# Optimization experiments

Measured on AMD Instinct MI355X. Metric: run time of the kernel, lower is better.

## Reference

```python
import jax, jax.numpy as jnp
import numpy as np
import math

B, T, F, H = 8, 1024, 512, 8
D = F // H  # 64
MIN_VAL = float(np.finfo(np.float32).min)


def setup_inputs() -> dict:
    key = jax.random.key(0)
    ks = jax.random.split(key, 16)
    w = lambda k, shape: jax.random.normal(k, shape, dtype=jnp.float32) * 0.02
    return {
        "query": jax.random.normal(ks[0], (B, T, F), dtype=jnp.float32),
        "key": jax.random.normal(ks[1], (B, T, F), dtype=jnp.float32),
        "value": jax.random.normal(ks[2], (B, T, F), dtype=jnp.float32),
        "mask": jax.random.randint(ks[3], (B, T, T), 0, 2, dtype=jnp.int32),
        "pos_emb": jax.random.normal(ks[4], (1, T, F), dtype=jnp.float32),
        "Wq": w(ks[5], (F, F)), "bq": jnp.zeros((F,), jnp.float32),
        "Wk": w(ks[6], (F, F)), "bk": jnp.zeros((F,), jnp.float32),
        "Wv": w(ks[7], (F, F)), "bv": jnp.zeros((F,), jnp.float32),
        "Wp": w(ks[8], (F, F)),
        "Wo": w(ks[9], (F, F)), "bo": jnp.zeros((F,), jnp.float32),
        "pos_bias_u": w(ks[10], (H, D)),
        "pos_bias_v": w(ks[11], (H, D)),
    }


def reference(query, key, value, mask, pos_emb, Wq, bq, Wk, bk, Wv, bv, Wp, Wo, bo, pos_bias_u, pos_bias_v):
    n_batch = query.shape[0]
    # projections (torch Linear: x @ W.T + b)
    q = (query @ Wq.T + bq).reshape(n_batch, -1, H, D)          # (B, T1, H, D)
    k = (key @ Wk.T + bk).reshape(n_batch, -1, H, D).transpose(0, 2, 1, 3)    # (B, H, T2, D)
    v = (value @ Wv.T + bv).reshape(n_batch, -1, H, D).transpose(0, 2, 1, 3)  # (B, H, T2, D)
    # relative position projection; pos_emb batch is 1 -> squeeze for broadcast
    p = (pos_emb @ Wp.T).reshape(pos_emb.shape[0], -1, H, D).transpose(0, 2, 1, 3)[0]  # (H, T2, D)

    q_u = q + pos_bias_u  # broadcast (H, D) over (B, T1, H, D)
    q_v = q + pos_bias_v
    matrix_ac = jnp.einsum("bthd,bhsd->bhts", q_u, k)
    matrix_bd = jnp.einsum("bthd,hsd->bhts", q_v, p)
    scores = (matrix_ac + matrix_bd) / math.sqrt(D)  # (B, H, T1, T2)

    m = (mask[:, None, :, :] == 0)  # (B, 1, T1, T2)
    scores = jnp.where(m, MIN_VAL, scores)
    attn = jnp.where(m, 0.0, jax.nn.softmax(scores, axis=-1))

    x = jnp.einsum("bhts,bhsd->bthd", attn, v).reshape(n_batch, -1, H * D)
    return x @ Wo.T + bo
```

## Files before the change

### kernel.cpp

```cpp
#include <hip/hip_runtime.h>

typedef float f32x4 __attribute__((ext_vector_type(4)));
typedef short bf16x8 __attribute__((ext_vector_type(8)));
typedef unsigned short u16x8 __attribute__((ext_vector_type(8)));

__device__ __forceinline__ unsigned short f2bf(float f) {
  union { float f; unsigned int u; } c; c.f = f;
  unsigned int r = (c.u + 0x7fffu + ((c.u >> 16) & 1u)) >> 16;
  return (unsigned short)r;
}
__device__ __forceinline__ float bf2f(unsigned short u) {
  union { unsigned int u; float f; } c; c.u = ((unsigned int)u) << 16;
  return c.f;
}

struct CvtWArgs {
  const float* s[5];
  unsigned short* d[5];
};

__global__ __launch_bounds__(256) void cvt_w(CvtWArgs a) {
  const int seg = blockIdx.y;
  const float* __restrict__ src = a.s[seg];
  unsigned short* __restrict__ dst = a.d[seg];
  int i = (blockIdx.x * 256 + threadIdx.x) * 8;
  float4 v0 = *(const float4*)&src[i];
  float4 v1 = *(const float4*)&src[i + 4];
  u16x8 o;
  o[0] = f2bf(v0.x); o[1] = f2bf(v0.y); o[2] = f2bf(v0.z); o[3] = f2bf(v0.w);
  o[4] = f2bf(v1.x); o[5] = f2bf(v1.y); o[6] = f2bf(v1.z); o[7] = f2bf(v1.w);
  *(u16x8*)&dst[i] = o;
}

__global__ __launch_bounds__(256) void pack_mask(const int* __restrict__ mask,
                                                 unsigned long long* __restrict__ bits) {
  size_t i = (size_t)blockIdx.x * 256 + threadIdx.x;
  unsigned long long b = __ballot(mask[i] != 0);
  if ((threadIdx.x & 63) == 0) bits[i >> 6] = b;
}

template <int IN_FP32, typename OT, int MODE>
__global__ __launch_bounds__(256) void proj_mfma(
    const void* __restrict__ Xv, const unsigned short* __restrict__ W,
    const float* __restrict__ bias, OT* __restrict__ out)
{
  __shared__ unsigned short AL[128 * 64];
  __shared__ unsigned short BL[64 * 64];
  const int tid = threadIdx.x;
  const int lane = tid & 63, wv = tid >> 6;
  const int lg = lane >> 4, lr = lane & 15;
  const int wm = wv >> 1, wn = wv & 1;
  const int row0 = blockIdx.x * 128, col0 = blockIdx.y * 64;

  f32x4 acc[4][2];
#pragma unroll
  for (int i = 0; i < 4; ++i)
#pragma unroll
    for (int j = 0; j < 2; ++j) { f32x4 z = {0.f,0.f,0.f,0.f}; acc[i][j] = z; }

  for (int k0 = 0; k0 < 512; k0 += 64) {
    __syncthreads();
    if constexpr (IN_FP32) {
      const float* X = (const float*)Xv;
#pragma unroll
      for (int j = 0; j < 4; ++j) {
        int idx = j * 256 + tid;
        int r = idx >> 3, u = idx & 7;
        const float* p = &X[(size_t)(row0 + r) * 512 + k0 + u * 8];
        float4 x0 = *(const float4*)p;
        float4 x1 = *(const float4*)(p + 4);
        u16x8 o;
        o[0] = f2bf(x0.x); o[1] = f2bf(x0.y); o[2] = f2bf(x0.z); o[3] = f2bf(x0.w);
        o[4] = f2bf(x1.x); o[5] = f2bf(x1.y); o[6] = f2bf(x1.z); o[7] = f2bf(x1.w);
        *(u16x8*)&AL[r * 64 + ((u ^ (r & 7)) << 3)] = o;
      }
    } else {
      const unsigned short* X = (const unsigned short*)Xv;
#pragma unroll
      for (int j = 0; j < 4; ++j) {
        int idx = j * 256 + tid;
        int r = idx >> 3, u = idx & 7;
        uint4 v = *(const uint4*)&X[(size_t)(row0 + r) * 512 + k0 + u * 8];
        *(uint4*)&AL[r * 64 + ((u ^ (r & 7)) << 3)] = v;
      }
    }
#pragma unroll
    for (int j = 0; j < 2; ++j) {
      int idx = j * 256 + tid;
      int r = idx >> 3, u = idx & 7;
      uint4 w = *(const uint4*)&W[(size_t)(col0 + r) * 512 + k0 + u * 8];
      *(uint4*)&BL[r * 64 + ((u ^ (r & 7)) << 3)] = w;
    }
    __syncthreads();

    bf16x8 af[4][2], bf[2][2];
#pragma unroll
    for (int mf = 0; mf < 4; ++mf)
#pragma unroll
      for (int ks = 0; ks < 2; ++ks) {
        int row = wm * 64 + mf * 16 + lr;
        af[mf][ks] = *(const bf16x8*)&AL[row * 64 + (((ks * 4 + lg) ^ (lr & 7)) << 3)];
      }
#pragma unroll
    for (int nf = 0; nf < 2; ++nf)
#pragma unroll
      for (int ks = 0; ks < 2; ++ks) {
        int col = wn * 32 + nf * 16 + lr;
        bf[nf][ks] = *(const bf16x8*)&BL[col * 64 + (((ks * 4 + lg) ^ (lr & 7)) << 3)];
      }
#pragma unroll
    for (int mf = 0; mf < 4; ++mf)
#pragma unroll
      for (int nf = 0; nf < 2; ++nf)
#pragma unroll
        for (int ks = 0; ks < 2; ++ks)
          acc[mf][nf] = __builtin_amdgcn_mfma_f32_16x16x32_bf16(
              af[mf][ks], bf[nf][ks], acc[mf][nf], 0, 0, 0);
  }

#pragma unroll
  for (int mf = 0; mf < 4; ++mf)
#pragma unroll
    for (int nf = 0; nf < 2; ++nf) {
      int col = col0 + wn * 32 + nf * 16 + lr;
      float bv = (bias != nullptr) ? bias[col] : 0.f;
#pragma unroll
      for (int reg = 0; reg < 4; ++reg) {
        int n = row0 + wm * 64 + mf * 16 + lg * 4 + reg;
        float val = acc[mf][nf][reg] + bv;
        if (MODE == 0) {
          int bI = n >> 10, t = n & 1023, hI = col >> 6, d = col & 63;
          size_t off = ((size_t)(bI * 8 + hI) * 1024 + t) * 64 + d;
          if constexpr (sizeof(OT) == 2) out[off] = (OT)f2bf(val);
          else out[off] = (OT)val;
        } else {
          out[(size_t)n * 512 + col] = (OT)val;
        }
      }
    }
}

__global__ __launch_bounds__(256) void attn_mfma(
    const unsigned short* __restrict__ Q, const unsigned short* __restrict__ K,
    const unsigned short* __restrict__ P, const unsigned short* __restrict__ V,
    const unsigned long long* __restrict__ bits,
    const float* __restrict__ ubias, const float* __restrict__ vbias,
    unsigned short* __restrict__ X)
{
  __shared__ unsigned short KL[64 * 128];
  __shared__ unsigned short VtL[64 * 64];
  __shared__ unsigned short PL[4 * 32 * 72];

  const int tid = threadIdx.x;
  const int lane = tid & 63, wq = tid >> 6;
  const int lg = lane >> 4, lr = lane & 15;
  const int bh = blockIdx.y, b = bh >> 3, h = bh & 7;
  const int tw = blockIdx.x * 128 + wq * 32;

  bf16x8 qa[2][4];
#pragma unroll
  for (int mf = 0; mf < 2; ++mf) {
    const unsigned short* qrow = Q + ((size_t)bh * 1024 + tw + mf * 16 + lr) * 64;
    uint4 qlo = *(const uint4*)&qrow[lg * 8];
    uint4 qhi = *(const uint4*)&qrow[32 + lg * 8];
#pragma unroll
    for (int ks = 0; ks < 4; ++ks) {
      int d0 = (ks & 1) * 32 + lg * 8;
      const float* bb = (ks < 2) ? (ubias + h * 64) : (vbias + h * 64);
      float4 b0 = *(const float4*)&bb[d0];
      float4 b1 = *(const float4*)&bb[d0 + 4];
      uint4 qq = (ks & 1) ? qhi : qlo;
      unsigned int qw[4] = {qq.x, qq.y, qq.z, qq.w};
      float bbv[8] = {b0.x, b0.y, b0.z, b0.w, b1.x, b1.y, b1.z, b1.w};
      bf16x8 a;
#pragma unroll
      for (int e = 0; e < 8; ++e) {
        unsigned short qb = (e & 1) ? (unsigned short)(qw[e >> 1] >> 16)
                                    : (unsigned short)(qw[e >> 1] & 0xffffu);
        a[e] = (short)f2bf((bf2f(qb) + bbv[e]) * 0.125f);
      }
      qa[mf][ks] = a;
    }
  }

  f32x4 Ofr[2][4];
  float m_[2][4], l_[2][4];
#pragma unroll
  for (int mf = 0; mf < 2; ++mf) {
#pragma unroll
    for (int nf = 0; nf < 4; ++nf) { f32x4 z = {0.f,0.f,0.f,0.f}; Ofr[mf][nf] = z; }
#pragma unroll
    for (int r = 0; r < 4; ++r) { m_[mf][r] = -3.4e38f; l_[mf][r] = 0.f; }
  }

  const unsigned short* Kg = K + (size_t)bh * 65536;
  const unsigned short* Pg = P + (size_t)h * 65536;
  const unsigned short* Vg = V + (size_t)bh * 65536;
  const unsigned long long* brow = bits + (size_t)b * 16384;
  unsigned short* Pl = PL + wq * (32 * 72);

  for (int s0t = 0; s0t < 16; ++s0t) {
    const int s0 = s0t * 64;
    __syncthreads();
#pragma unroll
    for (int j = 0; j < 4; ++j) {
      int idx = j * 256 + tid;
      int r = idx >> 4, c = idx & 15;
      uint4 v = (c < 8) ? *(const uint4*)&Kg[(size_t)(s0 + r) * 64 + c * 8]
                        : *(const uint4*)&Pg[(size_t)(s0 + r) * 64 + (c - 8) * 8];
      *(uint4*)&KL[r * 128 + ((c ^ (r & 7)) << 3)] = v;
    }
#pragma unroll
    for (int j = 0; j < 2; ++j) {
      int idx = j * 256 + tid;
      int s = idx >> 3, dc = idx & 7;
      uint4 v = *(const uint4*)&Vg[(size_t)(s0 + s) * 64 + dc * 8];
      unsigned int w[4] = {v.x, v.y, v.z, v.w};
#pragma unroll
      for (int e = 0; e < 8; ++e) {
        int d = dc * 8 + e;
        unsigned short val = (e & 1) ? (unsigned short)(w[e >> 1] >> 16)
                                     : (unsigned short)(w[e >> 1] & 0xffffu);
        VtL[d * 64 + (((s >> 3) ^ (d & 7)) << 3) + (s & 7)] = val;
      }
    }
    __syncthreads();

    unsigned long long mw[2][4];
#pragma unroll
    for (int mf = 0; mf < 2; ++mf)
#pragma unroll
      for (int r = 0; r < 4; ++r)
        mw[mf][r] = brow[(size_t)(tw + mf * 16 + lg * 4 + r) * 16 + s0t];

    f32x4 S[2][4];
#pragma unroll
    for (int nf = 0; nf < 4; ++nf) {
      bf16x8 kb[4];
#pragma unroll
      for (int ks = 0; ks < 4; ++ks)
        kb[ks] = *(const bf16x8*)&KL[(nf * 16 + lr) * 128 + (((ks * 4 + lg) ^ (lr & 7)) << 3)];
#pragma unroll
      for (int mf = 0; mf < 2; ++mf) {
        f32x4 a = {0.f, 0.f, 0.f, 0.f};
#pragma unroll
        for (int ks = 0; ks < 4; ++ks)
          a = __builtin_amdgcn_mfma_f32_16x16x32_bf16(qa[mf][ks], kb[ks], a, 0, 0, 0);
        S[mf][nf] = a;
      }
    }

#pragma unroll
    for (int mf = 0; mf < 2; ++mf)
#pragma unroll
      for (int r = 0; r < 4; ++r) {
        float v = fmaxf(fmaxf(S[mf][0][r], S[mf][1][r]), fmaxf(S[mf][2][r], S[mf][3][r]));
        v = fmaxf(v, __shfl_xor(v, 1));
        v = fmaxf(v, __shfl_xor(v, 2));
        v = fmaxf(v, __shfl_xor(v, 4));
        v = fmaxf(v, __shfl_xor(v, 8));
        float mo = m_[mf][r];
        float mn = fmaxf(mo, v);
        m_[mf][r] = mn;
        float sc = __expf(mo - mn);
        l_[mf][r] *= sc;
#pragma unroll
        for (int nf = 0; nf < 4; ++nf) Ofr[mf][nf][r] *= sc;
        float ps = 0.f;
#pragma unroll
        for (int nf = 0; nf < 4; ++nf) {
          float e = __expf(S[mf][nf][r] - mn);
          e = ((mw[mf][r] >> (nf * 16 + lr)) & 1ull) ? e : 0.f;
          S[mf][nf][r] = e;
          ps += e;
        }
        ps += __shfl_xor(ps, 1);
        ps += __shfl_xor(ps, 2);
        ps += __shfl_xor(ps, 4);
        ps += __shfl_xor(ps, 8);
        l_[mf][r] += ps;
      }

#pragma unroll
    for (int mf = 0; mf < 2; ++mf)
#pragma unroll
      for (int nf = 0; nf < 4; ++nf)
#pragma unroll
        for (int r = 0; r < 4; ++r)
          Pl[(mf * 16 + lg * 4 + r) * 72 + nf * 16 + lr] = f2bf(S[mf][nf][r]);
    __syncthreads();

    bf16x8 pa[2][2];
#pragma unroll
    for (int mf = 0; mf < 2; ++mf)
#pragma unroll
      for (int k2 = 0; k2 < 2; ++k2)
        pa[mf][k2] = *(const bf16x8*)&Pl[(mf * 16 + lr) * 72 + k2 * 32 + lg * 8];
#pragma unroll
    for (int nf2 = 0; nf2 < 4; ++nf2) {
      int d = nf2 * 16 + lr;
      bf16x8 vb[2];
#pragma unroll
      for (int k2 = 0; k2 < 2; ++k2)
        vb[k2] = *(const bf16x8*)&VtL[d * 64 + (((k2 * 4 + lg) ^ (d & 7)) << 3)];
#pragma unroll
      for (int mf = 0; mf < 2; ++mf)
#pragma unroll
        for (int k2 = 0; k2 < 2; ++k2)
          Ofr[mf][nf2] = __builtin_amdgcn_mfma_f32_16x16x32_bf16(
              pa[mf][k2], vb[k2], Ofr[mf][nf2], 0, 0, 0);
    }
  }

#pragma unroll
  for (int mf = 0; mf < 2; ++mf)
#pragma unroll
    for (int r = 0; r < 4; ++r) {
      float l = l_[mf][r];
      float inv = (l > 0.f) ? 1.f / l : 0.f;
      int t = tw + mf * 16 + lg * 4 + r;
#pragma unroll
      for (int nf2 = 0; nf2 < 4; ++nf2)
        X[((size_t)b * 1024 + t) * 512 + h * 64 + nf2 * 16 + lr] =
            f2bf(Ofr[mf][nf2][r] * inv);
    }
}

extern "C" void kernel_launch(void* const* d_in, const int* in_sizes, int n_in,
                              void* d_out, int out_size, void* d_ws, size_t ws_size,
                              hipStream_t stream) {
  const float* query = (const float*)d_in[0];
  const float* key   = (const float*)d_in[1];
  const float* value = (const float*)d_in[2];
  const int*   mask  = (const int*)d_in[3];
  const float* pos   = (const float*)d_in[4];
  const float* Wq = (const float*)d_in[5];
  const float* bq = (const float*)d_in[6];
  const float* Wk = (const float*)d_in[7];
  const float* bk = (const float*)d_in[8];
  const float* Wv = (const float*)d_in[9];
  const float* bv = (const float*)d_in[10];
  const float* Wp = (const float*)d_in[11];
  const float* Wo = (const float*)d_in[12];
  const float* bo = (const float*)d_in[13];
  const float* ub = (const float*)d_in[14];
  const float* vb = (const float*)d_in[15];
  float* out = (float*)d_out;

  char* w = (char*)d_ws;
  auto alloc = [&](size_t bytes) {
    char* p = w; w += (bytes + 255) & ~(size_t)255; return p;
  };
  const size_t NA = (size_t)8 * 1024 * 512;
  const size_t NW = (size_t)512 * 512;
  const size_t NP = (size_t)1024 * 512;

  unsigned short* wsQ = (unsigned short*)alloc(NA * 2);
  unsigned short* wsK = (unsigned short*)alloc(NA * 2);
  unsigned short* wsV = (unsigned short*)alloc(NA * 2);
  unsigned short* wsP = (unsigned short*)alloc(NP * 2);
  unsigned short* wsX = (unsigned short*)alloc(NA * 2);
  unsigned long long* bitsW = (unsigned long long*)alloc((size_t)8 * 1024 * 16 * 8);
  unsigned short* Wqb = (unsigned short*)alloc(NW * 2);
  unsigned short* Wkb = (unsigned short*)alloc(NW * 2);
  unsigned short* Wvb = (unsigned short*)alloc(NW * 2);
  unsigned short* Wpb = (unsigned short*)alloc(NW * 2);
  unsigned short* Wob = (unsigned short*)alloc(NW * 2);

  CvtWArgs ca;
  ca.s[0] = Wq; ca.d[0] = Wqb;
  ca.s[1] = Wk; ca.d[1] = Wkb;
  ca.s[2] = Wv; ca.d[2] = Wvb;
  ca.s[3] = Wp; ca.d[3] = Wpb;
  ca.s[4] = Wo; ca.d[4] = Wob;

  dim3 blk(256);
  cvt_w<<<dim3(128, 5), blk, 0, stream>>>(ca);
  pack_mask<<<dim3(32768), blk, 0, stream>>>(mask, bitsW);
  proj_mfma<1, unsigned short, 0><<<dim3(64, 8), blk, 0, stream>>>(query, Wqb, bq, wsQ);
  proj_mfma<1, unsigned short, 0><<<dim3(64, 8), blk, 0, stream>>>(key,   Wkb, bk, wsK);
  proj_mfma<1, unsigned short, 0><<<dim3(64, 8), blk, 0, stream>>>(value, Wvb, bv, wsV);
  proj_mfma<1, unsigned short, 0><<<dim3(8, 8),  blk, 0, stream>>>(pos,   Wpb, nullptr, wsP);
  attn_mfma<<<dim3(8, 64), blk, 0, stream>>>(wsQ, wsK, wsP, wsV, bitsW, ub, vb, wsX);
  proj_mfma<0, float, 1><<<dim3(64, 8), blk, 0, stream>>>(wsX, Wob, bo, out);
}
```

Baseline: 313.7 us.

## Write V pre-transposed from projection, halve attention rows per wave, widen projection blocks

The V projection gains an epilogue mode that stages its output through shared memory and writes V already transposed (d-major per head). This lets the attention kernel load V tiles with plain vector copies instead of scattering single elements into shared memory. The attention kernel now gives each wave 16 query rows instead of 32 and launches twice as many blocks, trading K/V tile reuse for more parallelism and fewer registers. Projection blocks go from 256 to 512 threads, so each wave holds fewer accumulators.

Result: no change. 310.3 us (-1.1%).

```diff
diff --git a/kernel.cpp b/kernel.cpp
--- a/kernel.cpp
+++ b/kernel.cpp
@@ -40,21 +40,22 @@
 }
 
 template <int IN_FP32, typename OT, int MODE>
-__global__ __launch_bounds__(256) void proj_mfma(
+__global__ __launch_bounds__(512) void proj_mfma(
     const void* __restrict__ Xv, const unsigned short* __restrict__ W,
     const float* __restrict__ bias, OT* __restrict__ out)
 {
-  __shared__ unsigned short AL[128 * 64];
-  __shared__ unsigned short BL[64 * 64];
+  __shared__ unsigned short SM[128 * 64 + 64 * 64];
+  unsigned short* AL = SM;
+  unsigned short* BL = SM + 128 * 64;
   const int tid = threadIdx.x;
   const int lane = tid & 63, wv = tid >> 6;
   const int lg = lane >> 4, lr = lane & 15;
   const int wm = wv >> 1, wn = wv & 1;
   const int row0 = blockIdx.x * 128, col0 = blockIdx.y * 64;
 
-  f32x4 acc[4][2];
-#pragma unroll
-  for (int i = 0; i < 4; ++i)
+  f32x4 acc[2][2];
+#pragma unroll
+  for (int i = 0; i < 2; ++i)
 #pragma unroll
     for (int j = 0; j < 2; ++j) { f32x4 z = {0.f,0.f,0.f,0.f}; acc[i][j] = z; }
 
@@ -63,8 +64,8 @@
     if constexpr (IN_FP32) {
       const float* X = (const float*)Xv;
 #pragma unroll
-      for (int j = 0; j < 4; ++j) {
-        int idx = j * 256 + tid;
+      for (int j = 0; j < 2; ++j) {
+        int idx = j * 512 + tid;
         int r = idx >> 3, u = idx & 7;
         const float* p = &X[(size_t)(row0 + r) * 512 + k0 + u * 8];
         float4 x0 = *(const float4*)p;
@@ -77,28 +78,26 @@
     } else {
       const unsigned short* X = (const unsigned short*)Xv;
 #pragma unroll
-      for (int j = 0; j < 4; ++j) {
-        int idx = j * 256 + tid;
+      for (int j = 0; j < 2; ++j) {
+        int idx = j * 512 + tid;
         int r = idx >> 3, u = idx & 7;
         uint4 v = *(const uint4*)&X[(size_t)(row0 + r) * 512 + k0 + u * 8];
         *(uint4*)&AL[r * 64 + ((u ^ (r & 7)) << 3)] = v;
       }
     }
-#pragma unroll
-    for (int j = 0; j < 2; ++j) {
-      int idx = j * 256 + tid;
-      int r = idx >> 3, u = idx & 7;
+    {
+      int r = tid >> 3, u = tid & 7;
       uint4 w = *(const uint4*)&W[(size_t)(col0 + r) * 512 + k0 + u * 8];
       *(uint4*)&BL[r * 64 + ((u ^ (r & 7)) << 3)] = w;
     }
     __syncthreads();
 
-    bf16x8 af[4][2], bf[2][2];
-#pragma unroll
-    for (int mf = 0; mf < 4; ++mf)
+    bf16x8 af[2][2], bf[2][2];
+#pragma unroll
+    for (int mf = 0; mf < 2; ++mf)
 #pragma unroll
       for (int ks = 0; ks < 2; ++ks) {
-        int row = wm * 64 + mf * 16 + lr;
+        int row = wm * 32 + mf * 16 + lr;
         af[mf][ks] = *(const bf16x8*)&AL[row * 64 + (((ks * 4 + lg) ^ (lr & 7)) << 3)];
       }
 #pragma unroll
@@ -109,7 +108,7 @@
         bf[nf][ks] = *(const bf16x8*)&BL[col * 64 + (((ks * 4 + lg) ^ (lr & 7)) << 3)];
       }
 #pragma unroll
-    for (int mf = 0; mf < 4; ++mf)
+    for (int mf = 0; mf < 2; ++mf)
 #pragma unroll
       for (int nf = 0; nf < 2; ++nf)
 #pragma unroll
@@ -118,49 +117,76 @@
               af[mf][ks], bf[nf][ks], acc[mf][nf], 0, 0, 0);
   }
 
-#pragma unroll
-  for (int mf = 0; mf < 4; ++mf)
-#pragma unroll
-    for (int nf = 0; nf < 2; ++nf) {
-      int col = col0 + wn * 32 + nf * 16 + lr;
-      float bv = (bias != nullptr) ? bias[col] : 0.f;
-#pragma unroll
-      for (int reg = 0; reg < 4; ++reg) {
-        int n = row0 + wm * 64 + mf * 16 + lg * 4 + reg;
-        float val = acc[mf][nf][reg] + bv;
-        if (MODE == 0) {
-          int bI = n >> 10, t = n & 1023, hI = col >> 6, d = col & 63;
-          size_t off = ((size_t)(bI * 8 + hI) * 1024 + t) * 64 + d;
-          if constexpr (sizeof(OT) == 2) out[off] = (OT)f2bf(val);
-          else out[off] = (OT)val;
-        } else {
-          out[(size_t)n * 512 + col] = (OT)val;
+  if constexpr (MODE == 2) {
+    unsigned short* TL = SM;
+    __syncthreads();
+#pragma unroll
+    for (int mf = 0; mf < 2; ++mf)
+#pragma unroll
+      for (int nf = 0; nf < 2; ++nf) {
+        int dl = wn * 32 + nf * 16 + lr;
+        float bv = bias[col0 + dl];
+#pragma unroll
+        for (int reg = 0; reg < 4; ++reg) {
+          int tl = wm * 32 + mf * 16 + lg * 4 + reg;
+          TL[tl * 73 + dl] = f2bf(acc[mf][nf][reg] + bv);
         }
       }
-    }
+    __syncthreads();
+    const int bI = row0 >> 10, hI = col0 >> 6, t0 = row0 & 1023;
+#pragma unroll
+    for (int j = 0; j < 2; ++j) {
+      int slot = j * 512 + tid;
+      int d = slot >> 4, ch = slot & 15;
+      u16x8 o;
+#pragma unroll
+      for (int e = 0; e < 8; ++e) o[e] = TL[(ch * 8 + e) * 73 + d];
+      *(u16x8*)&out[((size_t)((bI * 8 + hI) * 64) + d) * 1024 + t0 + ch * 8] = o;
+    }
+  } else {
+#pragma unroll
+    for (int mf = 0; mf < 2; ++mf)
+#pragma unroll
+      for (int nf = 0; nf < 2; ++nf) {
+        int col = col0 + wn * 32 + nf * 16 + lr;
+        float bv = (bias != nullptr) ? bias[col] : 0.f;
+#pragma unroll
+        for (int reg = 0; reg < 4; ++reg) {
+          int n = row0 + wm * 32 + mf * 16 + lg * 4 + reg;
+          float val = acc[mf][nf][reg] + bv;
+          if (MODE == 0) {
+            int bI = n >> 10, t = n & 1023, hI = col >> 6, d = col & 63;
+            size_t off = ((size_t)(bI * 8 + hI) * 1024 + t) * 64 + d;
+            if constexpr (sizeof(OT) == 2) out[off] = (OT)f2bf(val);
+            else out[off] = (OT)val;
+          } else {
+            out[(size_t)n * 512 + col] = (OT)val;
+          }
+        }
+      }
+  }
 }
 
 __global__ __launch_bounds__(256) void attn_mfma(
     const unsigned short* __restrict__ Q, const unsigned short* __restrict__ K,
-    const unsigned short* __restrict__ P, const unsigned short* __restrict__ V,
+    const unsigned short* __restrict__ P, const unsigned short* __restrict__ Vt,
     const unsigned long long* __restrict__ bits,
     const float* __restrict__ ubias, const float* __restrict__ vbias,
     unsigned short* __restrict__ X)
 {
   __shared__ unsigned short KL[64 * 128];
   __shared__ unsigned short VtL[64 * 64];
-  __shared__ unsigned short PL[4 * 32 * 72];
+  __shared__ unsigned short PL[4 * 16 * 72];
 
   const int tid = threadIdx.x;
   const int lane = tid & 63, wq = tid >> 6;
   const int lg = lane >> 4, lr = lane & 15;
   const int bh = blockIdx.y, b = bh >> 3, h = bh & 7;
-  const int tw = blockIdx.x * 128 + wq * 32;
-
-  bf16x8 qa[2][4];
-#pragma unroll
-  for (int mf = 0; mf < 2; ++mf) {
-    const unsigned short* qrow = Q + ((size_t)bh * 1024 + tw + mf * 16 + lr) * 64;
+  const int tw = blockIdx.x * 64 + wq * 16;
+
+  bf16x8 qa[4];
+  {
+    const unsigned short* qrow = Q + ((size_t)bh * 1024 + tw + lr) * 64;
     uint4 qlo = *(const uint4*)&qrow[lg * 8];
     uint4 qhi = *(const uint4*)&qrow[32 + lg * 8];
 #pragma unroll
@@ -179,25 +205,22 @@
                                     : (unsigned short)(qw[e >> 1] & 0xffffu);
         a[e] = (short)f2bf((bf2f(qb) + bbv[e]) * 0.125f);
       }
-      qa[mf][ks] = a;
-    }
-  }
-
-  f32x4 Ofr[2][4];
-  float m_[2][4], l_[2][4];
-#pragma unroll
-  for (int mf = 0; mf < 2; ++mf) {
-#pragma unroll
-    for (int nf = 0; nf < 4; ++nf) { f32x4 z = {0.f,0.f,0.f,0.f}; Ofr[mf][nf] = z; }
-#pragma unroll
-    for (int r = 0; r < 4; ++r) { m_[mf][r] = -3.4e38f; l_[mf][r] = 0.f; }
-  }
+      qa[ks] = a;
+    }
+  }
+
+  f32x4 Ofr[4];
+  float m_[4], l_[4];
+#pragma unroll
+  for (int nf = 0; nf < 4; ++nf) { f32x4 z = {0.f,0.f,0.f,0.f}; Ofr[nf] = z; }
+#pragma unroll
+  for (int r = 0; r < 4; ++r) { m_[r] = -3.4e38f; l_[r] = 0.f; }
 
   const unsigned short* Kg = K + (size_t)bh * 65536;
   const unsigned short* Pg = P + (size_t)h * 65536;
-  const unsigned short* Vg = V + (size_t)bh * 65536;
+  const unsigned short* Vg = Vt + (size_t)bh * 65536;
   const unsigned long long* brow = bits + (size_t)b * 16384;
-  unsigned short* Pl = PL + wq * (32 * 72);
+  unsigned short* Pl = PL + wq * (16 * 72);
 
   for (int s0t = 0; s0t < 16; ++s0t) {
     const int s0 = s0t * 64;
@@ -213,89 +236,71 @@
 #pragma unroll
     for (int j = 0; j < 2; ++j) {
       int idx = j * 256 + tid;
-      int s = idx >> 3, dc = idx & 7;
-      uint4 v = *(const uint4*)&Vg[(size_t)(s0 + s) * 64 + dc * 8];
-      unsigned int w[4] = {v.x, v.y, v.z, v.w};
-#pragma unroll
-      for (int e = 0; e < 8; ++e) {
-        int d = dc * 8 + e;
-        unsigned short val = (e & 1) ? (unsigned short)(w[e >> 1] >> 16)
-                                     : (unsigned short)(w[e >> 1] & 0xffffu);
-        VtL[d * 64 + (((s >> 3) ^ (d & 7)) << 3) + (s & 7)] = val;
-      }
-    }
-    __syncthreads();
-
-    unsigned long long mw[2][4];
-#pragma unroll
-    for (int mf = 0; mf < 2; ++mf)
-#pragma unroll
-      for (int r = 0; r < 4; ++r)
-        mw[mf][r] = brow[(size_t)(tw + mf * 16 + lg * 4 + r) * 16 + s0t];
-
-    f32x4 S[2][4];
+      int d = idx >> 3, u = idx & 7;
+      uint4 v = *(const uint4*)&Vg[(size_t)d * 1024 + s0 + u * 8];
+      *(uint4*)&VtL[d * 64 + ((u ^ (d & 7)) << 3)] = v;
+    }
+    __syncthreads();
+
+    unsigned long long mw[4];
+#pragma unroll
+    for (int r = 0; r < 4; ++r)
+      mw[r] = brow[(size_t)(tw + lg * 4 + r) * 16 + s0t];
+
+    f32x4 S[4];
 #pragma unroll
     for (int nf = 0; nf < 4; ++nf) {
       bf16x8 kb[4];
 #pragma unroll
       for (int ks = 0; ks < 4; ++ks)
         kb[ks] = *(const bf16x8*)&KL[(nf * 16 + lr) * 128 + (((ks * 4 + lg) ^ (lr & 7)) << 3)];
-#pragma unroll
-      for (int mf = 0; mf < 2; ++mf) {
-        f32x4 a = {0.f, 0.f, 0.f, 0.f};
-#pragma unroll
-        for (int ks = 0; ks < 4; ++ks)
-          a = __builtin_amdgcn_mfma_f32_16x16x32_bf16(qa[mf][ks], kb[ks], a, 0, 0, 0);
-        S[mf][nf] = a;
-      }
-    }
-
-#pragma unroll
-    for (int mf = 0; mf < 2; ++mf)
-#pragma unroll
-      for (int r = 0; r < 4; ++r) {
-        float v = fmaxf(fmaxf(S[mf][0][r], S[mf][1][r]), fmaxf(S[mf][2][r], S[mf][3][r]));
-        v = fmaxf(v, __shfl_xor(v, 1));
-        v = fmaxf(v, __shfl_xor(v, 2));
-        v = fmaxf(v, __shfl_xor(v, 4));
-        v = fmaxf(v, __shfl_xor(v, 8));
-        float mo = m_[mf][r];
-        float mn = fmaxf(mo, v);
-        m_[mf][r] = mn;
-        float sc = __expf(mo - mn);
-        l_[mf][r] *= sc;
-#pragma unroll
-        for (int nf = 0; nf < 4; ++nf) Ofr[mf][nf][r] *= sc;
-        float ps = 0.f;
-#pragma unroll
-        for (int nf = 0; nf < 4; ++nf) {
-          float e = __expf(S[mf][nf][r] - mn);
-          e = ((mw[mf][r] >> (nf * 16 + lr)) & 1ull) ? e : 0.f;
-          S[mf][nf][r] = e;
-          ps += e;
-        }
-        ps += __shfl_xor(ps, 1);
-        ps += __shfl_xor(ps, 2);
-        ps += __shfl_xor(ps, 4);
-        ps += __shfl_xor(ps, 8);
-        l_[mf][r] += ps;
-      }
-
-#pragma unroll
-    for (int mf = 0; mf < 2; ++mf)
-#pragma unroll
-      for (int nf = 0; nf < 4; ++nf)
-#pragma unroll
-        for (int r = 0; r < 4; ++r)
-          Pl[(mf * 16 + lg * 4 + r) * 72 + nf * 16 + lr] = f2bf(S[mf][nf][r]);
-    __syncthreads();
-
-    bf16x8 pa[2][2];
-#pragma unroll
-    for (int mf = 0; mf < 2; ++mf)
-#pragma unroll
-      for (int k2 = 0; k2 < 2; ++k2)
-        pa[mf][k2] = *(const bf16x8*)&Pl[(mf * 16 + lr) * 72 + k2 * 32 + lg * 8];
+      f32x4 a = {0.f, 0.f, 0.f, 0.f};
+#pragma unroll
+      for (int ks = 0; ks < 4; ++ks)
+        a = __builtin_amdgcn_mfma_f32_16x16x32_bf16(qa[ks], kb[ks], a, 0, 0, 0);
+      S[nf] = a;
+    }
+
+#pragma unroll
+    for (int r = 0; r < 4; ++r) {
+      float v = fmaxf(fmaxf(S[0][r], S[1][r]), fmaxf(S[2][r], S[3][r]));
+      v = fmaxf(v, __shfl_xor(v, 1));
+      v = fmaxf(v, __shfl_xor(v, 2));
+      v = fmaxf(v, __shfl_xor(v, 4));
+      v = fmaxf(v, __shfl_xor(v, 8));
+      float mo = m_[r];
+      float mn = fmaxf(mo, v);
+      m_[r] = mn;
+      float sc = __expf(mo - mn);
+      l_[r] *= sc;
+#pragma unroll
+      for (int nf = 0; nf < 4; ++nf) Ofr[nf][r] *= sc;
+      float ps = 0.f;
+#pragma unroll
+      for (int nf = 0; nf < 4; ++nf) {
+        float e = __expf(S[nf][r] - mn);
+        e = ((mw[r] >> (nf * 16 + lr)) & 1ull) ? e : 0.f;
+        S[nf][r] = e;
+        ps += e;
+      }
+      ps += __shfl_xor(ps, 1);
+      ps += __shfl_xor(ps, 2);
+      ps += __shfl_xor(ps, 4);
+      ps += __shfl_xor(ps, 8);
+      l_[r] += ps;
+    }
+
+#pragma unroll
+    for (int nf = 0; nf < 4; ++nf)
+#pragma unroll
+      for (int r = 0; r < 4; ++r)
+        Pl[(lg * 4 + r) * 72 + nf * 16 + lr] = f2bf(S[nf][r]);
+    __syncthreads();
+
+    bf16x8 pa[2];
+#pragma unroll
+    for (int k2 = 0; k2 < 2; ++k2)
+      pa[k2] = *(const bf16x8*)&Pl[lr * 72 + k2 * 32 + lg * 8];
 #pragma unroll
     for (int nf2 = 0; nf2 < 4; ++nf2) {
       int d = nf2 * 16 + lr;
@@ -304,26 +309,22 @@
       for (int k2 = 0; k2 < 2; ++k2)
         vb[k2] = *(const bf16x8*)&VtL[d * 64 + (((k2 * 4 + lg) ^ (d & 7)) << 3)];
 #pragma unroll
-      for (int mf = 0; mf < 2; ++mf)
-#pragma unroll
-        for (int k2 = 0; k2 < 2; ++k2)
-          Ofr[mf][nf2] = __builtin_amdgcn_mfma_f32_16x16x32_bf16(
-              pa[mf][k2], vb[k2], Ofr[mf][nf2], 0, 0, 0);
-    }
-  }
-
-#pragma unroll
-  for (int mf = 0; mf < 2; ++mf)
-#pragma unroll
-    for (int r = 0; r < 4; ++r) {
-      float l = l_[mf][r];
-      float inv = (l > 0.f) ? 1.f / l : 0.f;
-      int t = tw + mf * 16 + lg * 4 + r;
-#pragma unroll
-      for (int nf2 = 0; nf2 < 4; ++nf2)
-        X[((size_t)b * 1024 + t) * 512 + h * 64 + nf2 * 16 + lr] =
-            f2bf(Ofr[mf][nf2][r] * inv);
-    }
+      for (int k2 = 0; k2 < 2; ++k2)
+        Ofr[nf2] = __builtin_amdgcn_mfma_f32_16x16x32_bf16(
+            pa[k2], vb[k2], Ofr[nf2], 0, 0, 0);
+    }
+  }
+
+#pragma unroll
+  for (int r = 0; r < 4; ++r) {
+    float l = l_[r];
+    float inv = (l > 0.f) ? 1.f / l : 0.f;
+    int t = tw + lg * 4 + r;
+#pragma unroll
+    for (int nf2 = 0; nf2 < 4; ++nf2)
+      X[((size_t)b * 1024 + t) * 512 + h * 64 + nf2 * 16 + lr] =
+          f2bf(Ofr[nf2][r] * inv);
+  }
 }
 
 extern "C" void kernel_launch(void* const* d_in, const int* in_sizes, int n_in,
@@ -355,11 +356,11 @@
   const size_t NW = (size_t)512 * 512;
   const size_t NP = (size_t)1024 * 512;
 
-  unsigned short* wsQ = (unsigned short*)alloc(NA * 2);
-  unsigned short* wsK = (unsigned short*)alloc(NA * 2);
-  unsigned short* wsV = (unsigned short*)alloc(NA * 2);
-  unsigned short* wsP = (unsigned short*)alloc(NP * 2);
-  unsigned short* wsX = (unsigned short*)alloc(NA * 2);
+  unsigned short* wsQ  = (unsigned short*)alloc(NA * 2);
+  unsigned short* wsK  = (unsigned short*)alloc(NA * 2);
+  unsigned short* wsVt = (unsigned short*)alloc(NA * 2);
+  unsigned short* wsP  = (unsigned short*)alloc(NP * 2);
+  unsigned short* wsX  = (unsigned short*)alloc(NA * 2);
   unsigned long long* bitsW = (unsigned long long*)alloc((size_t)8 * 1024 * 16 * 8);
   unsigned short* Wqb = (unsigned short*)alloc(NW * 2);
   unsigned short* Wkb = (unsigned short*)alloc(NW * 2);
@@ -374,13 +375,12 @@
   ca.s[3] = Wp; ca.d[3] = Wpb;
   ca.s[4] = Wo; ca.d[4] = Wob;
 
-  dim3 blk(256);
-  cvt_w<<<dim3(128, 5), blk, 0, stream>>>(ca);
-  pack_mask<<<dim3(32768), blk, 0, stream>>>(mask, bitsW);
-  proj_mfma<1, unsigned short, 0><<<dim3(64, 8), blk, 0, stream>>>(query, Wqb, bq, wsQ);
-  proj_mfma<1, unsigned short, 0><<<dim3(64, 8), blk, 0, stream>>>(key,   Wkb, bk, wsK);
-  proj_mfma<1, unsigned short, 0><<<dim3(64, 8), blk, 0, stream>>>(value, Wvb, bv, wsV);
-  proj_mfma<1, unsigned short, 0><<<dim3(8, 8),  blk, 0, stream>>>(pos,   Wpb, nullptr, wsP);
-  attn_mfma<<<dim3(8, 64), blk, 0, stream>>>(wsQ, wsK, wsP, wsV, bitsW, ub, vb, wsX);
-  proj_mfma<0, float, 1><<<dim3(64, 8), blk, 0, stream>>>(wsX, Wob, bo, out);
-}
+  cvt_w<<<dim3(128, 5), dim3(256), 0, stream>>>(ca);
+  pack_mask<<<dim3(32768), dim3(256), 0, stream>>>(mask, bitsW);
+  proj_mfma<1, unsigned short, 0><<<dim3(64, 8), dim3(512), 0, stream>>>(query, Wqb, bq, wsQ);
+  proj_mfma<1, unsigned short, 0><<<dim3(64, 8), dim3(512), 0, stream>>>(key,   Wkb, bk, wsK);
+  proj_mfma<1, unsigned short, 2><<<dim3(64, 8), dim3(512), 0, stream>>>(value, Wvb, bv, wsVt);
+  proj_mfma<1, unsigned short, 0><<<dim3(8, 8),  dim3(512), 0, stream>>>(pos,   Wpb, nullptr, wsP);
+  attn_mfma<<<dim3(16, 64), dim3(256), 0, stream>>>(wsQ, wsK, wsP, wsVt, bitsW, ub, vb, wsX);
+  proj_mfma<0, float, 1><<<dim3(64, 8), dim3(512), 0, stream>>>(wsX, Wob, bo, out);
+}
```
